# Kernel tuning notes

Measured on AMD Instinct MI355X. Metric: run time of the kernel, lower is better.

## Reference

```python
import jax, jax.numpy as jnp
import numpy as np

N, D, C = 4096, 512, 64
MARGIN = 1.0
INF = jnp.float32(1e30)


def setup_inputs() -> dict:
    key = jax.random.key(0)
    k1, k2 = jax.random.split(key)
    embeddings = jax.random.normal(k1, (N, D), dtype=jnp.float32)
    targets = jax.random.randint(k2, (N,), 0, C)
    return {"embeddings": embeddings, "targets": targets}


def _triplet_loss(embeddings, targets, margin=MARGIN):
    # Squared pairwise distances [N, N] (differentiable, used for the loss)
    sq_norms = jnp.sum(embeddings * embeddings, axis=1)
    sq_dist = jnp.maximum(
        sq_norms[:, None] + sq_norms[None, :] - 2.0 * (embeddings @ embeddings.T), 0.0
    )
    # Euclidean distances for mining only (index selection is non-differentiable in torch)
    dist = jnp.sqrt(jax.lax.stop_gradient(sq_dist))

    same = targets[:, None] == targets[None, :]  # [N, N] same-label mask

    # Hardest negative per anchor: argmax_k (d_ap - d_ak + margin) == argmin_k d_ak over negatives
    neg_dist = jnp.where(same, INF, dist)
    n_idx = jnp.argmin(neg_dist, axis=1)   # [N] hardest negative index per anchor
    min_neg = jnp.min(neg_dist, axis=1)    # [N] its euclidean distance

    idx = jnp.arange(dist.shape[0])
    # anchor-positive pairs: same label, a < p (torch.combinations on sorted indices)
    pair_mask = same & (idx[:, None] < idx[None, :])
    # triplet kept only if mined loss (euclidean) strictly positive
    valid = pair_mask & (dist - min_neg[:, None] + margin > 0)

    ap_sq = sq_dist                         # [N, N] squared anchor-positive distances
    an_sq = sq_dist[idx, n_idx]             # [N]   squared anchor-hard-negative distances
    losses = jax.nn.relu(ap_sq - an_sq[:, None] + margin)

    cnt = jnp.sum(valid)
    denom = jnp.maximum(cnt, 1).astype(losses.dtype)
    loss = jnp.sum(jnp.where(valid, losses, 0.0)) / denom

    correct = jnp.sum(valid & (ap_sq < an_sq[:, None]))
    accuracy = correct.astype(jnp.float32) / jnp.maximum(cnt, 1).astype(jnp.float32)
    return loss, accuracy


def reference(embeddings, targets):
    return _triplet_loss(embeddings, targets)
```

## Files before the change

kernel.cpp:

```cpp
#include <hip/hip_runtime.h>

#define N 4096
#define D 512
#define C 64
#define MARGIN 1.0f
#define TILE 64
#define BK 64
#define ROWB 128
#define NTILES (N / TILE)
#define NTRI (NTILES * (NTILES + 1) / 2)
#define FINF 3.0e38f
#define MAXM 112
#define SKB 144
#define SLOTW 16

typedef __attribute__((ext_vector_type(8))) short short8;
typedef __attribute__((ext_vector_type(4))) float floatx4;

__device__ __forceinline__ unsigned short f2bf(float f) {
  unsigned int u = __float_as_uint(f);
  u += 0x7FFFu + ((u >> 16) & 1u);
  return (unsigned short)(u >> 16);
}

__device__ __forceinline__ void gload_lds16(const void* g, void* l) {
  __builtin_amdgcn_global_load_lds(
      (const __attribute__((address_space(1))) unsigned int*)g,
      (__attribute__((address_space(3))) unsigned int*)l, 16, 0, 0);
}

__global__ __launch_bounds__(256) void prep_kernel(const float* __restrict__ E,
                                                   const int* __restrict__ targets,
                                                   unsigned short* __restrict__ Ebf,
                                                   float* __restrict__ norms,
                                                   unsigned int* __restrict__ an_sq_bits,
                                                   int* __restrict__ cls_mem,
                                                   int* __restrict__ cls_off,
                                                   unsigned int* __restrict__ done) {
  const int row = blockIdx.x;
  const int tid = threadIdx.x;
  if (row == N) {
    __shared__ unsigned int cnt[C];
    __shared__ unsigned int base[C];
    if (tid == 0) *done = 0u;
    if (tid < C) cnt[tid] = 0;
    __syncthreads();
    for (int i = tid; i < N; i += 256) atomicAdd(&cnt[targets[i]], 1);
    __syncthreads();
    if (tid == 0) {
      unsigned int s = 0;
      for (int c = 0; c < C; c++) { base[c] = s; s += cnt[c]; }
    }
    __syncthreads();
    if (tid < C) cnt[tid] = base[tid];
    __syncthreads();
    for (int i = tid; i < N; i += 256) {
      const int c = targets[i];
      const unsigned int p = atomicAdd(&cnt[c], 1);
      cls_mem[p] = i;
    }
    if (tid < C) cls_off[tid] = (int)base[tid];
    if (tid == 0) cls_off[C] = N;
    return;
  }
  if (row < 16) an_sq_bits[row * 256 + tid] = 0x7F800000u;
  const float2 v = reinterpret_cast<const float2*>(E + (size_t)row * D)[tid];
  float s = v.x * v.x + v.y * v.y;
  unsigned int packed = ((unsigned int)f2bf(v.y) << 16) | (unsigned int)f2bf(v.x);
  reinterpret_cast<unsigned int*>(Ebf + (size_t)row * D)[tid] = packed;
  for (int off = 32; off > 0; off >>= 1) s += __shfl_down(s, off);
  __shared__ float wsum[4];
  if ((tid & 63) == 0) wsum[tid >> 6] = s;
  __syncthreads();
  if (tid == 0) norms[row] = wsum[0] + wsum[1] + wsum[2] + wsum[3];
}

__global__ __launch_bounds__(256, 6) void gemm_min_kernel(const unsigned short* __restrict__ Ebf,
                                                          const float* __restrict__ norms,
                                                          const int* __restrict__ targets,
                                                          unsigned int* __restrict__ an_sq_bits) {
  const int u = blockIdx.x;
  int i = (int)((sqrtf(8.0f * (float)u + 1.0f) - 1.0f) * 0.5f);
  while ((i + 1) * (i + 2) / 2 <= u) ++i;
  while (i * (i + 1) / 2 > u) --i;
  const int tm = u - i * (i + 1) / 2;
  const int tn = i;

  __shared__ alignas(16) unsigned char As[TILE * ROWB];
  __shared__ alignas(16) unsigned char Bs[TILE * ROWB];
  __shared__ float s_rmin[2][TILE];
  __shared__ float s_cmin[2][TILE];

  const int tid = threadIdx.x;
  const int wave = tid >> 6, lane = tid & 63;
  const int quad = lane >> 4, l16 = lane & 15;
  const int wr = wave >> 1, wc = wave & 1;
  const int rowBase = tm * TILE, colBase = tn * TILE;

  const int lr = lane >> 3;
  const int lq = (lane & 7) ^ lr;
  const int lofs = lr * (D * 2) + lq * 16;
  const unsigned char* gA = (const unsigned char*)Ebf + (size_t)rowBase * (D * 2);
  const unsigned char* gB = (const unsigned char*)Ebf + (size_t)colBase * (D * 2);

  const int swz = l16 & 7;
  int rA[2], rB[2], cq[2];
#pragma unroll
  for (int s = 0; s < 2; s++) {
    rA[s] = (wr * 32 + s * 16 + l16) * ROWB;
    rB[s] = (wc * 32 + s * 16 + l16) * ROWB;
  }
#pragma unroll
  for (int ks = 0; ks < 2; ks++) cq[ks] = ((ks * 4 + quad) ^ swz) * 16;

  floatx4 acc[2][2];
#pragma unroll
  for (int a = 0; a < 2; a++)
#pragma unroll
    for (int b = 0; b < 2; b++) acc[a][b] = (floatx4){0.f, 0.f, 0.f, 0.f};

  for (int k0b = 0; k0b < D * 2; k0b += BK * 2) {
#pragma unroll
    for (int t = 0; t < 2; t++) {
      const int g = wave + t * 4;
      gload_lds16(gA + (size_t)g * 8 * (D * 2) + lofs + k0b, As + g * 1024);
      gload_lds16(gB + (size_t)g * 8 * (D * 2) + lofs + k0b, Bs + g * 1024);
    }
    __syncthreads();
#pragma unroll
    for (int ks = 0; ks < 2; ks++) {
      const short8 af0 = *reinterpret_cast<const short8*>(As + rA[0] + cq[ks]);
      const short8 af1 = *reinterpret_cast<const short8*>(As + rA[1] + cq[ks]);
      const short8 bf0 = *reinterpret_cast<const short8*>(Bs + rB[0] + cq[ks]);
      const short8 bf1 = *reinterpret_cast<const short8*>(Bs + rB[1] + cq[ks]);
      acc[0][0] = __builtin_amdgcn_mfma_f32_16x16x32_bf16(af0, bf0, acc[0][0], 0, 0, 0);
      acc[0][1] = __builtin_amdgcn_mfma_f32_16x16x32_bf16(af0, bf1, acc[0][1], 0, 0, 0);
      acc[1][0] = __builtin_amdgcn_mfma_f32_16x16x32_bf16(af1, bf0, acc[1][0], 0, 0, 0);
      acc[1][1] = __builtin_amdgcn_mfma_f32_16x16x32_bf16(af1, bf1, acc[1][1], 0, 0, 0);
    }
    __syncthreads();
  }

  int tcol[2];
  float ncol[2];
#pragma unroll
  for (int sn = 0; sn < 2; sn++) {
    const int gc = colBase + wc * 32 + sn * 16 + l16;
    tcol[sn] = targets[gc];
    ncol[sn] = norms[gc];
  }
  float colmin[2] = {FINF, FINF};
#pragma unroll
  for (int sm = 0; sm < 2; sm++) {
#pragma unroll
    for (int r = 0; r < 4; r++) {
      const int rloc = wr * 32 + sm * 16 + quad * 4 + r;
      const int grow = rowBase + rloc;
      const int trow = targets[grow];
      const float nrow = norms[grow];
      float rowmin = FINF;
#pragma unroll
      for (int sn = 0; sn < 2; sn++) {
        const float sq = fmaxf(nrow + ncol[sn] - 2.0f * acc[sm][sn][r], 0.0f);
        if (tcol[sn] != trow) {
          rowmin = fminf(rowmin, sq);
          colmin[sn] = fminf(colmin[sn], sq);
        }
      }
#pragma unroll
      for (int off = 1; off < 16; off <<= 1) rowmin = fminf(rowmin, __shfl_xor(rowmin, off));
      if (l16 == 0) s_rmin[wc][rloc] = rowmin;
    }
  }
#pragma unroll
  for (int sn = 0; sn < 2; sn++) {
    float cm = colmin[sn];
    cm = fminf(cm, __shfl_xor(cm, 16));
    cm = fminf(cm, __shfl_xor(cm, 32));
    if (quad == 0) s_cmin[wr][wc * 32 + sn * 16 + l16] = cm;
  }
  __syncthreads();
  if (tid < TILE) {
    const float m = fminf(s_rmin[0][tid], s_rmin[1][tid]);
    if (m < FINF) atomicMin(&an_sq_bits[rowBase + tid], __float_as_uint(m));
  } else if (tid < 2 * TILE) {
    const int c = tid - TILE;
    const float m = fminf(s_cmin[0][c], s_cmin[1][c]);
    if (m < FINF) atomicMin(&an_sq_bits[colBase + c], __float_as_uint(m));
  }
}

__global__ __launch_bounds__(256) void loss_kernel(const unsigned short* __restrict__ Ebf,
                                                   const float* __restrict__ norms,
                                                   const unsigned int* __restrict__ an_sq_bits,
                                                   const int* __restrict__ cls_mem,
                                                   const int* __restrict__ cls_off,
                                                   float* __restrict__ accs,
                                                   unsigned int* __restrict__ done,
                                                   float* __restrict__ out) {
  const int c = blockIdx.x;
  const int tid = threadIdx.x, wave = tid >> 6, lane = tid & 63;
  const int quad = lane >> 4, l16 = lane & 15;
  const int o = cls_off[c];
  const int s_c = min(cls_off[c + 1] - o, MAXM);

  __shared__ alignas(16) unsigned char S[MAXM * SKB];
  __shared__ int l_mem[MAXM];
  __shared__ float l_norm[MAXM];
  __shared__ float l_an[MAXM];
  __shared__ signed char pti[28], ptj[28];
  __shared__ float s_sum[4];
  __shared__ unsigned int s_cnt[4], s_cor[4];
  __shared__ int s_last;

  if (tid < s_c) {
    const int m = cls_mem[o + tid];
    l_mem[tid] = m;
    l_norm[tid] = norms[m];
    l_an[tid] = __uint_as_float(an_sq_bits[m]);
  }
  const int nt = (s_c + 15) >> 4;
  const int npairs = nt * (nt + 1) / 2;
  if (tid == 0) {
    int w = 0;
    for (int ti = 0; ti < nt; ti++)
      for (int tj = ti; tj < nt; tj++) { pti[w] = (signed char)ti; ptj[w] = (signed char)tj; w++; }
  }
  __syncthreads();

  floatx4 pacc[7];
#pragma unroll
  for (int pp = 0; pp < 7; pp++) pacc[pp] = (floatx4){0.f, 0.f, 0.f, 0.f};

  for (int k0 = 0; k0 < D; k0 += BK) {
    for (int s = tid; s < s_c * 8; s += 256) {
      const int r = s >> 3, q = s & 7;
      *reinterpret_cast<uint4*>(&S[r * SKB + q * 16]) =
          *reinterpret_cast<const uint4*>(&Ebf[(size_t)l_mem[r] * D + k0 + q * 8]);
    }
    __syncthreads();
#pragma unroll
    for (int pp = 0; pp < 7; pp++) {
      const int p = wave + 4 * pp;
      if (p < npairs) {
        const int ti = pti[p], tj = ptj[p];
#pragma unroll
        for (int ks = 0; ks < 2; ks++) {
          const short8 af = *reinterpret_cast<const short8*>(&S[(ti * 16 + l16) * SKB + ks * 64 + quad * 16]);
          const short8 bf = *reinterpret_cast<const short8*>(&S[(tj * 16 + l16) * SKB + ks * 64 + quad * 16]);
          pacc[pp] = __builtin_amdgcn_mfma_f32_16x16x32_bf16(af, bf, pacc[pp], 0, 0, 0);
        }
      }
    }
    __syncthreads();
  }

  float bsum = 0.f;
  unsigned int bcnt = 0, bcor = 0;
#pragma unroll
  for (int pp = 0; pp < 7; pp++) {
    const int p = wave + 4 * pp;
    if (p < npairs) {
      const int ti = pti[p], tj = ptj[p];
#pragma unroll
      for (int r = 0; r < 4; r++) {
        const int i_loc = ti * 16 + quad * 4 + r;
        const int j_loc = tj * 16 + l16;
        if (i_loc < s_c && j_loc < s_c && (ti < tj || i_loc < j_loc)) {
          const int oi = l_mem[i_loc], oj = l_mem[j_loc];
          const float sq = fmaxf(l_norm[i_loc] + l_norm[j_loc] - 2.0f * pacc[pp][r], 0.0f);
          const float an = (oi < oj) ? l_an[i_loc] : l_an[j_loc];
          if (sqrtf(sq) - sqrtf(an) + MARGIN > 0.0f) {
            bcnt++;
            bsum += fmaxf(sq - an + MARGIN, 0.0f);
            if (sq < an) bcor++;
          }
        }
      }
    }
  }
#pragma unroll
  for (int off = 32; off > 0; off >>= 1) {
    bsum += __shfl_down(bsum, off);
    bcnt += __shfl_down(bcnt, off);
    bcor += __shfl_down(bcor, off);
  }
  if (lane == 0) { s_sum[wave] = bsum; s_cnt[wave] = bcnt; s_cor[wave] = bcor; }
  __syncthreads();
  if (tid == 0) {
    float* slot = accs + (size_t)c * SLOTW;
    atomicExch((unsigned int*)&slot[0], __float_as_uint(s_sum[0] + s_sum[1] + s_sum[2] + s_sum[3]));
    atomicExch((unsigned int*)&slot[1], s_cnt[0] + s_cnt[1] + s_cnt[2] + s_cnt[3]);
    atomicExch((unsigned int*)&slot[2], s_cor[0] + s_cor[1] + s_cor[2] + s_cor[3]);
    __threadfence();
    s_last = (atomicAdd(done, 1u) == C - 1);
  }
  __syncthreads();
  if (s_last) {
    __threadfence();
    if (tid < C) {
      float sum = __uint_as_float(atomicAdd((unsigned int*)&accs[(size_t)tid * SLOTW + 0], 0u));
      unsigned int cnt = atomicAdd((unsigned int*)&accs[(size_t)tid * SLOTW + 1], 0u);
      unsigned int cor = atomicAdd((unsigned int*)&accs[(size_t)tid * SLOTW + 2], 0u);
#pragma unroll
      for (int off = 32; off > 0; off >>= 1) {
        sum += __shfl_down(sum, off);
        cnt += __shfl_down(cnt, off);
        cor += __shfl_down(cor, off);
      }
      if (tid == 0) {
        const float denom = (float)(cnt > 0u ? cnt : 1u);
        out[0] = sum / denom;
        out[1] = (float)cor / denom;
      }
    }
  }
}

extern "C" void kernel_launch(void* const* d_in, const int* in_sizes, int n_in,
                              void* d_out, int out_size, void* d_ws, size_t ws_size,
                              hipStream_t stream) {
  const float* E = (const float*)d_in[0];
  const int* targets = (const int*)d_in[1];
  float* out = (float*)d_out;
  char* ws = (char*)d_ws;
  size_t off = 0;
  unsigned short* Ebf = (unsigned short*)(ws + off); off += (size_t)N * D * 2;
  float* norms = (float*)(ws + off); off += (size_t)N * 4;
  unsigned int* an_sq = (unsigned int*)(ws + off); off += (size_t)N * 4;
  float* accs = (float*)(ws + off); off += (size_t)C * SLOTW * 4;
  int* cls_mem = (int*)(ws + off); off += (size_t)N * 4;
  int* cls_off = (int*)(ws + off); off += 512;
  unsigned int* done = (unsigned int*)(ws + off);

  prep_kernel<<<dim3(N + 1), dim3(256), 0, stream>>>(E, targets, Ebf, norms, an_sq, cls_mem, cls_off, done);
  gemm_min_kernel<<<dim3(NTRI), dim3(256), 0, stream>>>(Ebf, norms, targets, an_sq);
  loss_kernel<<<dim3(C), dim3(256), 0, stream>>>(Ebf, norms, an_sq, cls_mem, cls_off, accs, done, out);
}
```

Measured before the change: 110.9 us.

## Enlarge GEMM tile to 128 and split loss kernel across pair groups

The distance-min GEMM now uses 128x128 tiles with a 4x4 MFMA block per wave, which raises data reuse and halves the number of triangular tiles and atomics, at the cost of more registers and lower occupancy (launch bounds 3). The loss kernel is spread over a second grid dimension of 7 groups per class, with each wave handling one 16x16 pair tile. Partial sums are combined with atomicAdd into accumulators that prep now zeroes. This adds parallelism to the small per-class kernel, but each group reloads the whole class embedding slice, which duplicates global loads.

```diff
diff --git a/kernel.cpp b/kernel.cpp
--- a/kernel.cpp
+++ b/kernel.cpp
@@ -4,8 +4,7 @@
 #define D 512
 #define C 64
 #define MARGIN 1.0f
-#define TILE 64
-#define BK 64
+#define TILE 128
 #define ROWB 128
 #define NTILES (N / TILE)
 #define NTRI (NTILES * (NTILES + 1) / 2)
@@ -13,6 +12,7 @@
 #define MAXM 112
 #define SKB 144
 #define SLOTW 16
+#define LOSS_G 7
 
 typedef __attribute__((ext_vector_type(8))) short short8;
 typedef __attribute__((ext_vector_type(4))) float floatx4;
@@ -36,6 +36,7 @@
                                                    unsigned int* __restrict__ an_sq_bits,
                                                    int* __restrict__ cls_mem,
                                                    int* __restrict__ cls_off,
+                                                   unsigned int* __restrict__ accs_u,
                                                    unsigned int* __restrict__ done) {
   const int row = blockIdx.x;
   const int tid = threadIdx.x;
@@ -43,6 +44,7 @@
     __shared__ unsigned int cnt[C];
     __shared__ unsigned int base[C];
     if (tid == 0) *done = 0u;
+    for (int k = tid; k < C * SLOTW; k += 256) accs_u[k] = 0u;
     if (tid < C) cnt[tid] = 0;
     __syncthreads();
     for (int i = tid; i < N; i += 256) atomicAdd(&cnt[targets[i]], 1);
@@ -75,7 +77,7 @@
   if (tid == 0) norms[row] = wsum[0] + wsum[1] + wsum[2] + wsum[3];
 }
 
-__global__ __launch_bounds__(256, 6) void gemm_min_kernel(const unsigned short* __restrict__ Ebf,
+__global__ __launch_bounds__(256, 3) void gemm_min_kernel(const unsigned short* __restrict__ Ebf,
                                                           const float* __restrict__ norms,
                                                           const int* __restrict__ targets,
                                                           unsigned int* __restrict__ an_sq_bits) {
@@ -104,63 +106,66 @@
   const unsigned char* gB = (const unsigned char*)Ebf + (size_t)colBase * (D * 2);
 
   const int swz = l16 & 7;
-  int rA[2], rB[2], cq[2];
-#pragma unroll
-  for (int s = 0; s < 2; s++) {
-    rA[s] = (wr * 32 + s * 16 + l16) * ROWB;
-    rB[s] = (wc * 32 + s * 16 + l16) * ROWB;
+  int rA[4], rB[4], cq[2];
+#pragma unroll
+  for (int s = 0; s < 4; s++) {
+    rA[s] = (wr * 64 + s * 16 + l16) * ROWB;
+    rB[s] = (wc * 64 + s * 16 + l16) * ROWB;
   }
 #pragma unroll
   for (int ks = 0; ks < 2; ks++) cq[ks] = ((ks * 4 + quad) ^ swz) * 16;
 
-  floatx4 acc[2][2];
-#pragma unroll
-  for (int a = 0; a < 2; a++)
-#pragma unroll
-    for (int b = 0; b < 2; b++) acc[a][b] = (floatx4){0.f, 0.f, 0.f, 0.f};
-
-  for (int k0b = 0; k0b < D * 2; k0b += BK * 2) {
-#pragma unroll
-    for (int t = 0; t < 2; t++) {
-      const int g = wave + t * 4;
+  floatx4 acc[4][4];
+#pragma unroll
+  for (int a = 0; a < 4; a++)
+#pragma unroll
+    for (int b = 0; b < 4; b++) acc[a][b] = (floatx4){0.f, 0.f, 0.f, 0.f};
+
+  for (int k0b = 0; k0b < D * 2; k0b += 128) {
+#pragma unroll
+    for (int t = 0; t < 4; t++) {
+      const int g = wave * 4 + t;
       gload_lds16(gA + (size_t)g * 8 * (D * 2) + lofs + k0b, As + g * 1024);
       gload_lds16(gB + (size_t)g * 8 * (D * 2) + lofs + k0b, Bs + g * 1024);
     }
     __syncthreads();
 #pragma unroll
     for (int ks = 0; ks < 2; ks++) {
-      const short8 af0 = *reinterpret_cast<const short8*>(As + rA[0] + cq[ks]);
-      const short8 af1 = *reinterpret_cast<const short8*>(As + rA[1] + cq[ks]);
-      const short8 bf0 = *reinterpret_cast<const short8*>(Bs + rB[0] + cq[ks]);
-      const short8 bf1 = *reinterpret_cast<const short8*>(Bs + rB[1] + cq[ks]);
-      acc[0][0] = __builtin_amdgcn_mfma_f32_16x16x32_bf16(af0, bf0, acc[0][0], 0, 0, 0);
-      acc[0][1] = __builtin_amdgcn_mfma_f32_16x16x32_bf16(af0, bf1, acc[0][1], 0, 0, 0);
-      acc[1][0] = __builtin_amdgcn_mfma_f32_16x16x32_bf16(af1, bf0, acc[1][0], 0, 0, 0);
-      acc[1][1] = __builtin_amdgcn_mfma_f32_16x16x32_bf16(af1, bf1, acc[1][1], 0, 0, 0);
-    }
-    __syncthreads();
-  }
-
-  int tcol[2];
-  float ncol[2];
-#pragma unroll
-  for (int sn = 0; sn < 2; sn++) {
-    const int gc = colBase + wc * 32 + sn * 16 + l16;
+      short8 af[4], bf[4];
+#pragma unroll
+      for (int s = 0; s < 4; s++) {
+        af[s] = *reinterpret_cast<const short8*>(As + rA[s] + cq[ks]);
+        bf[s] = *reinterpret_cast<const short8*>(Bs + rB[s] + cq[ks]);
+      }
+#pragma unroll
+      for (int sm = 0; sm < 4; sm++)
+#pragma unroll
+        for (int sn = 0; sn < 4; sn++)
+          acc[sm][sn] = __builtin_amdgcn_mfma_f32_16x16x32_bf16(af[sm], bf[sn], acc[sm][sn], 0, 0, 0);
+    }
+    __syncthreads();
+  }
+
+  int tcol[4];
+  float ncol[4];
+#pragma unroll
+  for (int sn = 0; sn < 4; sn++) {
+    const int gc = colBase + wc * 64 + sn * 16 + l16;
     tcol[sn] = targets[gc];
     ncol[sn] = norms[gc];
   }
-  float colmin[2] = {FINF, FINF};
-#pragma unroll
-  for (int sm = 0; sm < 2; sm++) {
+  float colmin[4] = {FINF, FINF, FINF, FINF};
+#pragma unroll
+  for (int sm = 0; sm < 4; sm++) {
 #pragma unroll
     for (int r = 0; r < 4; r++) {
-      const int rloc = wr * 32 + sm * 16 + quad * 4 + r;
+      const int rloc = wr * 64 + sm * 16 + quad * 4 + r;
       const int grow = rowBase + rloc;
       const int trow = targets[grow];
       const float nrow = norms[grow];
       float rowmin = FINF;
 #pragma unroll
-      for (int sn = 0; sn < 2; sn++) {
+      for (int sn = 0; sn < 4; sn++) {
         const float sq = fmaxf(nrow + ncol[sn] - 2.0f * acc[sm][sn][r], 0.0f);
         if (tcol[sn] != trow) {
           rowmin = fminf(rowmin, sq);
@@ -173,17 +178,17 @@
     }
   }
 #pragma unroll
-  for (int sn = 0; sn < 2; sn++) {
+  for (int sn = 0; sn < 4; sn++) {
     float cm = colmin[sn];
     cm = fminf(cm, __shfl_xor(cm, 16));
     cm = fminf(cm, __shfl_xor(cm, 32));
-    if (quad == 0) s_cmin[wr][wc * 32 + sn * 16 + l16] = cm;
+    if (quad == 0) s_cmin[wr][wc * 64 + sn * 16 + l16] = cm;
   }
   __syncthreads();
   if (tid < TILE) {
     const float m = fminf(s_rmin[0][tid], s_rmin[1][tid]);
     if (m < FINF) atomicMin(&an_sq_bits[rowBase + tid], __float_as_uint(m));
-  } else if (tid < 2 * TILE) {
+  } else {
     const int c = tid - TILE;
     const float m = fminf(s_cmin[0][c], s_cmin[1][c]);
     if (m < FINF) atomicMin(&an_sq_bits[colBase + c], __float_as_uint(m));
@@ -198,77 +203,68 @@
                                                    float* __restrict__ accs,
                                                    unsigned int* __restrict__ done,
                                                    float* __restrict__ out) {
-  const int c = blockIdx.x;
+  const int c = blockIdx.x, g = blockIdx.y;
   const int tid = threadIdx.x, wave = tid >> 6, lane = tid & 63;
   const int quad = lane >> 4, l16 = lane & 15;
   const int o = cls_off[c];
   const int s_c = min(cls_off[c + 1] - o, MAXM);
+  const int nt = (s_c + 15) >> 4;
+  const int npairs = nt * (nt + 1) / 2;
+  const bool active = (g * 4 < npairs);
 
   __shared__ alignas(16) unsigned char S[MAXM * SKB];
   __shared__ int l_mem[MAXM];
   __shared__ float l_norm[MAXM];
   __shared__ float l_an[MAXM];
-  __shared__ signed char pti[28], ptj[28];
   __shared__ float s_sum[4];
   __shared__ unsigned int s_cnt[4], s_cor[4];
   __shared__ int s_last;
 
-  if (tid < s_c) {
-    const int m = cls_mem[o + tid];
-    l_mem[tid] = m;
-    l_norm[tid] = norms[m];
-    l_an[tid] = __uint_as_float(an_sq_bits[m]);
-  }
-  const int nt = (s_c + 15) >> 4;
-  const int npairs = nt * (nt + 1) / 2;
-  if (tid == 0) {
-    int w = 0;
-    for (int ti = 0; ti < nt; ti++)
-      for (int tj = ti; tj < nt; tj++) { pti[w] = (signed char)ti; ptj[w] = (signed char)tj; w++; }
-  }
-  __syncthreads();
-
-  floatx4 pacc[7];
-#pragma unroll
-  for (int pp = 0; pp < 7; pp++) pacc[pp] = (floatx4){0.f, 0.f, 0.f, 0.f};
-
-  for (int k0 = 0; k0 < D; k0 += BK) {
-    for (int s = tid; s < s_c * 8; s += 256) {
-      const int r = s >> 3, q = s & 7;
-      *reinterpret_cast<uint4*>(&S[r * SKB + q * 16]) =
-          *reinterpret_cast<const uint4*>(&Ebf[(size_t)l_mem[r] * D + k0 + q * 8]);
-    }
-    __syncthreads();
-#pragma unroll
-    for (int pp = 0; pp < 7; pp++) {
-      const int p = wave + 4 * pp;
-      if (p < npairs) {
-        const int ti = pti[p], tj = ptj[p];
+  if (active) {
+    if (tid < s_c) {
+      const int m = cls_mem[o + tid];
+      l_mem[tid] = m;
+      l_norm[tid] = norms[m];
+      l_an[tid] = __uint_as_float(an_sq_bits[m]);
+    }
+    __syncthreads();
+    const int p = g * 4 + wave;
+    const bool havep = p < npairs;
+    int ti = 0, tj = 0;
+    if (havep) {
+      int pp = p, t = 0;
+      while (pp >= nt - t) { pp -= nt - t; t++; }
+      ti = t; tj = t + pp;
+    }
+    floatx4 pacc = (floatx4){0.f, 0.f, 0.f, 0.f};
+    for (int k0 = 0; k0 < D; k0 += 64) {
+      for (int s = tid; s < s_c * 8; s += 256) {
+        const int r = s >> 3, q = s & 7;
+        *reinterpret_cast<uint4*>(&S[r * SKB + q * 16]) =
+            *reinterpret_cast<const uint4*>(&Ebf[(size_t)l_mem[r] * D + k0 + q * 8]);
+      }
+      __syncthreads();
+      if (havep) {
 #pragma unroll
         for (int ks = 0; ks < 2; ks++) {
           const short8 af = *reinterpret_cast<const short8*>(&S[(ti * 16 + l16) * SKB + ks * 64 + quad * 16]);
           const short8 bf = *reinterpret_cast<const short8*>(&S[(tj * 16 + l16) * SKB + ks * 64 + quad * 16]);
-          pacc[pp] = __builtin_amdgcn_mfma_f32_16x16x32_bf16(af, bf, pacc[pp], 0, 0, 0);
+          pacc = __builtin_amdgcn_mfma_f32_16x16x32_bf16(af, bf, pacc, 0, 0, 0);
         }
       }
-    }
-    __syncthreads();
-  }
-
-  float bsum = 0.f;
-  unsigned int bcnt = 0, bcor = 0;
-#pragma unroll
-  for (int pp = 0; pp < 7; pp++) {
-    const int p = wave + 4 * pp;
-    if (p < npairs) {
-      const int ti = pti[p], tj = ptj[p];
+      __syncthreads();
+    }
+
+    float bsum = 0.f;
+    unsigned int bcnt = 0, bcor = 0;
+    if (havep) {
 #pragma unroll
       for (int r = 0; r < 4; r++) {
         const int i_loc = ti * 16 + quad * 4 + r;
         const int j_loc = tj * 16 + l16;
         if (i_loc < s_c && j_loc < s_c && (ti < tj || i_loc < j_loc)) {
           const int oi = l_mem[i_loc], oj = l_mem[j_loc];
-          const float sq = fmaxf(l_norm[i_loc] + l_norm[j_loc] - 2.0f * pacc[pp][r], 0.0f);
+          const float sq = fmaxf(l_norm[i_loc] + l_norm[j_loc] - 2.0f * pacc[r], 0.0f);
           const float an = (oi < oj) ? l_an[i_loc] : l_an[j_loc];
           if (sqrtf(sq) - sqrtf(an) + MARGIN > 0.0f) {
             bcnt++;
@@ -278,22 +274,25 @@
         }
       }
     }
-  }
-#pragma unroll
-  for (int off = 32; off > 0; off >>= 1) {
-    bsum += __shfl_down(bsum, off);
-    bcnt += __shfl_down(bcnt, off);
-    bcor += __shfl_down(bcor, off);
-  }
-  if (lane == 0) { s_sum[wave] = bsum; s_cnt[wave] = bcnt; s_cor[wave] = bcor; }
+#pragma unroll
+    for (int off = 32; off > 0; off >>= 1) {
+      bsum += __shfl_down(bsum, off);
+      bcnt += __shfl_down(bcnt, off);
+      bcor += __shfl_down(bcor, off);
+    }
+    if (lane == 0) { s_sum[wave] = bsum; s_cnt[wave] = bcnt; s_cor[wave] = bcor; }
+    __syncthreads();
+    if (tid == 0) {
+      float* slot = accs + (size_t)c * SLOTW;
+      atomicAdd(&slot[0], s_sum[0] + s_sum[1] + s_sum[2] + s_sum[3]);
+      atomicAdd((unsigned int*)&slot[1], s_cnt[0] + s_cnt[1] + s_cnt[2] + s_cnt[3]);
+      atomicAdd((unsigned int*)&slot[2], s_cor[0] + s_cor[1] + s_cor[2] + s_cor[3]);
+    }
+  }
   __syncthreads();
   if (tid == 0) {
-    float* slot = accs + (size_t)c * SLOTW;
-    atomicExch((unsigned int*)&slot[0], __float_as_uint(s_sum[0] + s_sum[1] + s_sum[2] + s_sum[3]));
-    atomicExch((unsigned int*)&slot[1], s_cnt[0] + s_cnt[1] + s_cnt[2] + s_cnt[3]);
-    atomicExch((unsigned int*)&slot[2], s_cor[0] + s_cor[1] + s_cor[2] + s_cor[3]);
     __threadfence();
-    s_last = (atomicAdd(done, 1u) == C - 1);
+    s_last = (atomicAdd(done, 1u) == (unsigned)(C * LOSS_G) - 1u);
   }
   __syncthreads();
   if (s_last) {
@@ -333,7 +332,9 @@
   int* cls_off = (int*)(ws + off); off += 512;
   unsigned int* done = (unsigned int*)(ws + off);
 
-  prep_kernel<<<dim3(N + 1), dim3(256), 0, stream>>>(E, targets, Ebf, norms, an_sq, cls_mem, cls_off, done);
+  prep_kernel<<<dim3(N + 1), dim3(256), 0, stream>>>(E, targets, Ebf, norms, an_sq, cls_mem,
+                                                     cls_off, (unsigned int*)accs, done);
   gemm_min_kernel<<<dim3(NTRI), dim3(256), 0, stream>>>(Ebf, norms, targets, an_sq);
-  loss_kernel<<<dim3(C), dim3(256), 0, stream>>>(Ebf, norms, an_sq, cls_mem, cls_off, accs, done, out);
-}
+  loss_kernel<<<dim3(C, LOSS_G), dim3(256), 0, stream>>>(Ebf, norms, an_sq, cls_mem, cls_off,
+                                                         accs, done, out);
+}
```

New measurement: 102.9 us. 1.08x faster.
